# Optimization experiments

Measured on AMD Instinct MI355X. Metric: run time of the kernel, lower is better.

Reference implementation:

```python
import jax, jax.numpy as jnp
import numpy as np

B, S, E, H = 4, 2048, 1024, 16
DK = E // H  # 64


def setup_inputs() -> dict:
    key = jax.random.key(0)
    ks = jax.random.split(key, 11)
    s_in = 1.0 / np.sqrt(E)
    return {
        "query": jax.random.normal(ks[0], (B, S, E), jnp.float32),
        "key_": jax.random.normal(ks[1], (B, S, E), jnp.float32),
        "value": jax.random.normal(ks[2], (B, S, E), jnp.float32),
        # nn.Linear weights stored as [out, in]; applied as x @ W.T + b
        "Wq": jax.random.uniform(ks[3], (E, E), jnp.float32, -s_in, s_in),
        "bq": jax.random.uniform(ks[4], (E,), jnp.float32, -s_in, s_in),
        "Wk": jax.random.uniform(ks[5], (E, E), jnp.float32, -s_in, s_in),
        "bk": jax.random.uniform(ks[6], (E,), jnp.float32, -s_in, s_in),
        "Wv": jax.random.uniform(ks[7], (E, E), jnp.float32, -s_in, s_in),
        "bv": jax.random.uniform(ks[8], (E,), jnp.float32, -s_in, s_in),
        "Wo": jax.random.uniform(ks[9], (E, E), jnp.float32, -s_in, s_in),
        "bo": jax.random.uniform(ks[10], (E,), jnp.float32, -s_in, s_in),
    }


def reference(query, key_, value, Wq, bq, Wk, bk, Wv, bv, Wo, bo):
    scale = 1.0 / np.sqrt(DK).astype(np.float32)
    Q = query @ Wq.T + bq   # [B,S,E]
    K = key_ @ Wk.T + bk
    V = value @ Wv.T + bv
    # split heads: [B,S,H,DK] (slicing dim -1 into contiguous per-head chunks)
    Qh = Q.reshape(B, S, H, DK)
    Kh = K.reshape(B, S, H, DK)
    Vh = V.reshape(B, S, H, DK)
    scores = jnp.einsum('bqhd,bkhd->bhqk', Qh, Kh) * scale  # [B,H,S,S]
    probs = jax.nn.softmax(scores, axis=-1)
    ctx = jnp.einsum('bhqk,bkhd->bqhd', probs, Vh).reshape(B, S, E)
    out = ctx @ Wo.T + bo
    return out
```

## Files before the change

kernel.cpp:

```cpp
#include <hip/hip_runtime.h>
#include <stdint.h>
#include <stddef.h>

constexpr int BB = 4, SS = 2048, EE = 1024, HH = 16, DKH = 64;
constexpr int MM = BB * SS;
constexpr float SM_SCALE_LOG2 = 0.18033688011112042f;

typedef unsigned short u16;
typedef __attribute__((ext_vector_type(8))) short bf16x8;
typedef __attribute__((ext_vector_type(8))) unsigned short u16x8;
typedef __attribute__((ext_vector_type(4))) float f32x4;
typedef __attribute__((ext_vector_type(16))) float f32x16;
typedef __attribute__((ext_vector_type(2))) unsigned int u32x2;
typedef __attribute__((ext_vector_type(4))) unsigned int u32x4;

__device__ __forceinline__ u16 f2bf(float f) {
  unsigned u = __builtin_bit_cast(unsigned, f);
  u += 0x7FFFu + ((u >> 16) & 1u);
  return (u16)(u >> 16);
}

__device__ __forceinline__ unsigned pack2(float lo, float hi) {
  unsigned r;
  asm("v_cvt_pk_bf16_f32 %0, %1, %2" : "=v"(r) : "v"(lo), "v"(hi));
  return r;
}

__device__ __forceinline__ void gld16(const void* g, void* l) {
  __builtin_amdgcn_global_load_lds(
      (const __attribute__((address_space(1))) unsigned int*)g,
      (__attribute__((address_space(3))) unsigned int*)l, 16, 0, 0);
}

struct Cvt3 { const float* in[3]; u16* out[3]; };
struct Cvt4 { const float* in[4]; u16* out[4]; };

__global__ void cvt_bf16_x3(Cvt3 p, int n8) {
  int i = blockIdx.x * 256 + threadIdx.x;
  if (i >= n8) return;
  const int z = blockIdx.y;
  const float4* src = (const float4*)p.in[z] + (size_t)i * 2;
  float4 a = src[0], b = src[1];
  u16x8 v;
  v[0] = f2bf(a.x); v[1] = f2bf(a.y); v[2] = f2bf(a.z); v[3] = f2bf(a.w);
  v[4] = f2bf(b.x); v[5] = f2bf(b.y); v[6] = f2bf(b.z); v[7] = f2bf(b.w);
  *((u16x8*)p.out[z] + i) = v;
}

__global__ void cvt_bf16_x4(Cvt4 p, int n8) {
  int i = blockIdx.x * 256 + threadIdx.x;
  if (i >= n8) return;
  const int z = blockIdx.y;
  const float4* src = (const float4*)p.in[z] + (size_t)i * 2;
  float4 a = src[0], b = src[1];
  u16x8 v;
  v[0] = f2bf(a.x); v[1] = f2bf(a.y); v[2] = f2bf(a.z); v[3] = f2bf(a.w);
  v[4] = f2bf(b.x); v[5] = f2bf(b.y); v[6] = f2bf(b.z); v[7] = f2bf(b.w);
  *((u16x8*)p.out[z] + i) = v;
}

struct GemmPtrs {
  const u16* A[3];
  const u16* W[3];
  const float* bias[3];
  void* C[3];
  float scale[3];
  int mode[3];
};

__global__ __launch_bounds__(256, 2) void gemm_bt(GemmPtrs p, int M, int N, int K) {
  __shared__ __align__(16) u16 As[2][128 * 32];
  __shared__ __align__(16) u16 Bs[2][128 * 32];
  const int t = threadIdx.x, l = t & 63, w = t >> 6;
  const int lm = l & 15, lg = l >> 4;
  const int wm = w >> 1, wn = w & 1;
  const int z = blockIdx.z;
  const u16* A = p.A[z];
  const u16* W = p.W[z];
  const float* bias = p.bias[z];
  const int m0 = blockIdx.y * 128, n0 = blockIdx.x * 128;
  const int wbase = (t & ~63) * 16;

  f32x4 acc[4][4];
  const f32x4 zero = {0.f, 0.f, 0.f, 0.f};
#pragma unroll
  for (int i = 0; i < 4; ++i)
#pragma unroll
    for (int j = 0; j < 4; ++j) acc[i][j] = zero;

  auto stage = [&](int buf, int kt) {
    const int k0 = kt * 32;
#pragma unroll
    for (int i = 0; i < 2; ++i) {
      const int slot = i * 256 + t;
      const int row = slot >> 2, c = slot & 3;
      gld16(A + (size_t)(m0 + row) * K + k0 + c * 8, (char*)&As[buf][0] + i * 4096 + wbase);
      gld16(W + (size_t)(n0 + row) * K + k0 + c * 8, (char*)&Bs[buf][0] + i * 4096 + wbase);
    }
  };

  stage(0, 0);
  __syncthreads();
  int cur = 0;
  const int NT = K >> 5;
  for (int kt = 0; kt < NT; ++kt) {
    if (kt + 1 < NT) stage(cur ^ 1, kt + 1);
    const u16* Ac = &As[cur][0];
    const u16* Bc = &Bs[cur][0];
    bf16x8 a[4], b[4];
#pragma unroll
    for (int i = 0; i < 4; ++i)
      a[i] = *(const bf16x8*)(Ac + (wm * 64 + i * 16 + lm) * 32 + lg * 8);
#pragma unroll
    for (int j = 0; j < 4; ++j)
      b[j] = *(const bf16x8*)(Bc + (wn * 64 + j * 16 + lm) * 32 + lg * 8);
#pragma unroll
    for (int i = 0; i < 4; ++i)
#pragma unroll
      for (int j = 0; j < 4; ++j)
        acc[i][j] = __builtin_amdgcn_mfma_f32_16x16x32_bf16(a[i], b[j], acc[i][j], 0, 0, 0);
    __syncthreads();
    cur ^= 1;
  }

  const float sc = p.scale[z];
  const int mode = p.mode[z];
#pragma unroll
  for (int i = 0; i < 4; ++i) {
    const int rbase = m0 + wm * 64 + i * 16 + lg * 4;
#pragma unroll
    for (int j = 0; j < 4; ++j) {
      const int col = n0 + wn * 64 + j * 16 + lm;
      const float bv = bias[col];
      float v[4];
#pragma unroll
      for (int r = 0; r < 4; ++r) v[r] = (acc[i][j][r] + bv) * sc;
      if (mode == 1) {
#pragma unroll
        for (int r = 0; r < 4; ++r)
          ((float*)p.C[z])[(size_t)(rbase + r) * N + col] = v[r];
      } else if (mode == 0) {
#pragma unroll
        for (int r = 0; r < 4; ++r)
          ((u16*)p.C[z])[(size_t)(rbase + r) * N + col] = f2bf(v[r]);
      } else {
        const int b = rbase >> 11, s = rbase & 2047;
        u16* dst = (u16*)p.C[z] +
                   ((size_t)((b * 16 + (col >> 6)) * 64 + (col & 63))) * SS + s;
        uint2 pk;
        pk.x = pack2(v[0], v[1]);
        pk.y = pack2(v[2], v[3]);
        *(uint2*)dst = pk;
      }
    }
  }
}

__global__ __launch_bounds__(256, 4) void attn_fwd3(const u16* __restrict__ Q,
                                                    const u16* __restrict__ K,
                                                    const u16* __restrict__ Vt,
                                                    u16* __restrict__ C) {
  __shared__ __align__(16) u16 Ks[2][64 * 64];
  __shared__ __align__(16) u16 Vs[2][64 * 64];

  const int t = threadIdx.x, l = t & 63, w = t >> 6;
  const int lq = l & 31, hi = l >> 5;
  const int q0 = blockIdx.x * 128;
  const int bh = blockIdx.y, bb = bh >> 4, hh = bh & 15;

  const u16* qp = Q + ((size_t)(bb * SS + q0 + w * 32 + lq)) * EE + hh * 64 + hi * 8;
  bf16x8 qf[4];
  qf[0] = *(const bf16x8*)(qp);
  qf[1] = *(const bf16x8*)(qp + 16);
  qf[2] = *(const bf16x8*)(qp + 32);
  qf[3] = *(const bf16x8*)(qp + 48);

  const u16* Kbase = K + (size_t)bb * SS * EE + hh * 64;
  const u16* Vbase = Vt + (size_t)bh * DKH * SS;

  f32x16 accA, accB;
  f32x16 z16;
#pragma unroll
  for (int i = 0; i < 16; ++i) { accA[i] = 0.f; accB[i] = 0.f; z16[i] = 0.f; }
  float lsum = 0.0f;

  auto stage = [&](int buf, int kt) {
#pragma unroll
    for (int i = 0; i < 2; ++i) {
      const int slot = i * 256 + t;
      const int row = slot >> 3, pc = slot & 7;
      const int lc = pc ^ (row & 7);
      const int lbyte = (i * 256 + (t & ~63)) * 16;
      gld16(Kbase + (size_t)(kt * 64 + row) * EE + lc * 8, (char*)&Ks[buf][0] + lbyte);
      gld16(Vbase + (size_t)row * SS + kt * 64 + lc * 8, (char*)&Vs[buf][0] + lbyte);
    }
  };

  auto mkfrag = [&](const f32x16& p, int base) -> bf16x8 {
    unsigned A0 = pack2(p[base + 0], p[base + 1]);
    unsigned A1 = pack2(p[base + 2], p[base + 3]);
    unsigned B0 = pack2(p[base + 4], p[base + 5]);
    unsigned B1 = pack2(p[base + 6], p[base + 7]);
    u32x2 r0 = __builtin_amdgcn_permlane32_swap(A0, B0, false, false);
    u32x2 r1 = __builtin_amdgcn_permlane32_swap(A1, B1, false, false);
    u32x4 fr;
    fr[0] = r0[0]; fr[1] = r1[0]; fr[2] = r0[1]; fr[3] = r1[1];
    return __builtin_bit_cast(bf16x8, fr);
  };

  stage(0, 0);
  __syncthreads();
  int cur = 0;
  for (int kt = 0; kt < SS / 64; ++kt) {
    if (kt + 1 < SS / 64) stage(cur ^ 1, kt + 1);
    const u16* Kc = &Ks[cur][0];
    const u16* Vc = &Vs[cur][0];

    f32x16 s0, s1;
    __builtin_amdgcn_s_setprio(1);
    {
      const int c = hi ^ (lq & 7);
      bf16x8 kf0 = *(const bf16x8*)(Kc + lq * 64 + c * 8);
      bf16x8 kf1 = *(const bf16x8*)(Kc + (32 + lq) * 64 + c * 8);
      s0 = __builtin_amdgcn_mfma_f32_32x32x16_bf16(kf0, qf[0], z16, 0, 0, 0);
      s1 = __builtin_amdgcn_mfma_f32_32x32x16_bf16(kf1, qf[0], z16, 0, 0, 0);
    }
#pragma unroll
    for (int m = 1; m < 4; ++m) {
      const int c = (2 * m + hi) ^ (lq & 7);
      bf16x8 kf0 = *(const bf16x8*)(Kc + lq * 64 + c * 8);
      bf16x8 kf1 = *(const bf16x8*)(Kc + (32 + lq) * 64 + c * 8);
      s0 = __builtin_amdgcn_mfma_f32_32x32x16_bf16(kf0, qf[m], s0, 0, 0, 0);
      s1 = __builtin_amdgcn_mfma_f32_32x32x16_bf16(kf1, qf[m], s1, 0, 0, 0);
    }
    __builtin_amdgcn_s_setprio(0);

#pragma unroll
    for (int i = 0; i < 16; ++i) {
      s0[i] = __builtin_amdgcn_exp2f(s0[i]);
      s1[i] = __builtin_amdgcn_exp2f(s1[i]);
    }
    float sa = 0.f, sb = 0.f, sc2 = 0.f, sd = 0.f;
#pragma unroll
    for (int i = 0; i < 8; ++i) {
      sa += s0[i]; sb += s0[i + 8];
      sc2 += s1[i]; sd += s1[i + 8];
    }
    lsum += (sa + sb) + (sc2 + sd);

    bf16x8 pf[4];
    pf[0] = mkfrag(s0, 0);
    pf[1] = mkfrag(s0, 8);
    pf[2] = mkfrag(s1, 0);
    pf[3] = mkfrag(s1, 8);

    __builtin_amdgcn_s_setprio(1);
#pragma unroll
    for (int s = 0; s < 4; ++s) {
      const int c = (2 * s + hi) ^ (lq & 7);
      bf16x8 vf0 = *(const bf16x8*)(Vc + lq * 64 + c * 8);
      bf16x8 vf1 = *(const bf16x8*)(Vc + (32 + lq) * 64 + c * 8);
      accA = __builtin_amdgcn_mfma_f32_32x32x16_bf16(vf0, pf[s], accA, 0, 0, 0);
      accB = __builtin_amdgcn_mfma_f32_32x32x16_bf16(vf1, pf[s], accB, 0, 0, 0);
    }
    __builtin_amdgcn_s_setprio(0);
    __syncthreads();
    cur ^= 1;
  }

  const float inv = 1.0f / (lsum + __shfl_xor(lsum, 32));
  char* Tw = (char*)&Ks[0][0] + w * 4096;
#pragma unroll
  for (int g = 0; g < 4; ++g) {
    uint2 pa, pb;
    pa.x = pack2(accA[4 * g + 0] * inv, accA[4 * g + 1] * inv);
    pa.y = pack2(accA[4 * g + 2] * inv, accA[4 * g + 3] * inv);
    pb.x = pack2(accB[4 * g + 0] * inv, accB[4 * g + 1] * inv);
    pb.y = pack2(accB[4 * g + 2] * inv, accB[4 * g + 3] * inv);
    const int sub = 8 * hi, sw = (lq & 7) << 4;
    *(uint2*)(Tw + lq * 128 + (((g) << 4) ^ sw) + sub) = pa;
    *(uint2*)(Tw + lq * 128 + (((4 + g) << 4) ^ sw) + sub) = pb;
  }
  const int qr0 = l >> 3, ch = l & 7;
#pragma unroll
  for (int ps = 0; ps < 4; ++ps) {
    const int qr = ps * 8 + qr0;
    u32x4 vv = *(const u32x4*)(Tw + qr * 128 + ((ch ^ (qr & 7)) << 4));
    u16* dst = C + ((size_t)(bb * SS + q0 + w * 32 + qr)) * EE + hh * 64 + ch * 8;
    *(u32x4*)dst = vv;
  }
}

extern "C" void kernel_launch(void* const* d_in, const int* in_sizes, int n_in,
                              void* d_out, int out_size, void* d_ws, size_t ws_size,
                              hipStream_t stream) {
  (void)in_sizes; (void)n_in; (void)out_size; (void)ws_size;
  const float* query = (const float*)d_in[0];
  const float* key_  = (const float*)d_in[1];
  const float* value = (const float*)d_in[2];
  const float* Wq = (const float*)d_in[3];
  const float* bq = (const float*)d_in[4];
  const float* Wk = (const float*)d_in[5];
  const float* bk = (const float*)d_in[6];
  const float* Wv = (const float*)d_in[7];
  const float* bv = (const float*)d_in[8];
  const float* Wo = (const float*)d_in[9];
  const float* bo = (const float*)d_in[10];

  char* ws = (char*)d_ws;
  const size_t SZX = (size_t)MM * EE * 2;
  const size_t SZW = (size_t)EE * EE * 2;
  u16* Xq  = (u16*)(ws + 0 * SZX);
  u16* Xk  = (u16*)(ws + 1 * SZX);
  u16* Xv  = (u16*)(ws + 2 * SZX);
  u16* Qb  = (u16*)(ws + 3 * SZX);
  u16* Kb  = (u16*)(ws + 4 * SZX);
  u16* Vtb = (u16*)(ws + 5 * SZX);
  u16* Cb  = (u16*)(ws + 6 * SZX);
  u16* Wqb = (u16*)(ws + 7 * SZX + 0 * SZW);
  u16* Wkb = (u16*)(ws + 7 * SZX + 1 * SZW);
  u16* Wvb = (u16*)(ws + 7 * SZX + 2 * SZW);
  u16* Wob = (u16*)(ws + 7 * SZX + 3 * SZW);

  const int n8x = MM * EE / 8;
  const int n8w = EE * EE / 8;

  Cvt3 cx{};
  cx.in[0] = query; cx.in[1] = key_; cx.in[2] = value;
  cx.out[0] = Xq; cx.out[1] = Xk; cx.out[2] = Xv;
  cvt_bf16_x3<<<dim3(n8x / 256, 3), 256, 0, stream>>>(cx, n8x);

  Cvt4 cw{};
  cw.in[0] = Wq; cw.in[1] = Wk; cw.in[2] = Wv; cw.in[3] = Wo;
  cw.out[0] = Wqb; cw.out[1] = Wkb; cw.out[2] = Wvb; cw.out[3] = Wob;
  cvt_bf16_x4<<<dim3(n8w / 256, 4), 256, 0, stream>>>(cw, n8w);

  GemmPtrs g{};
  g.A[0] = Xq; g.A[1] = Xk; g.A[2] = Xv;
  g.W[0] = Wqb; g.W[1] = Wkb; g.W[2] = Wvb;
  g.bias[0] = bq; g.bias[1] = bk; g.bias[2] = bv;
  g.C[0] = Qb; g.C[1] = Kb; g.C[2] = Vtb;
  g.scale[0] = SM_SCALE_LOG2; g.scale[1] = 1.0f; g.scale[2] = 1.0f;
  g.mode[0] = 0; g.mode[1] = 0; g.mode[2] = 2;
  gemm_bt<<<dim3(EE / 128, MM / 128, 3), 256, 0, stream>>>(g, MM, EE, EE);

  attn_fwd3<<<dim3(SS / 128, BB * HH), 256, 0, stream>>>(Qb, Kb, Vtb, Cb);

  GemmPtrs g2{};
  g2.A[0] = Cb; g2.W[0] = Wob; g2.bias[0] = bo; g2.C[0] = d_out;
  g2.scale[0] = 1.0f; g2.mode[0] = 1;
  gemm_bt<<<dim3(EE / 128, MM / 128, 1), 256, 0, stream>>>(g2, MM, EE, EE);
}
```

Before: 224.9 us.

## Replace projection GEMM with 256x256 tile, triple-buffered, swizzled LDS kernel

```diff
diff --git a/kernel.cpp b/kernel.cpp
--- a/kernel.cpp
+++ b/kernel.cpp
@@ -68,23 +68,29 @@
   int mode[3];
 };
 
-__global__ __launch_bounds__(256, 2) void gemm_bt(GemmPtrs p, int M, int N, int K) {
-  __shared__ __align__(16) u16 As[2][128 * 32];
-  __shared__ __align__(16) u16 Bs[2][128 * 32];
-  const int t = threadIdx.x, l = t & 63, w = t >> 6;
+__global__ __launch_bounds__(512, 2) void gemm256(GemmPtrs p, int M, int N, int K) {
+  __shared__ __align__(16) u16 SA[3][256 * 32];
+  __shared__ __align__(16) u16 SB[3][256 * 32];
+  const int t = threadIdx.x, l = t & 63;
+  const int w = t >> 6;
   const int lm = l & 15, lg = l >> 4;
-  const int wm = w >> 1, wn = w & 1;
+  const int wm = w >> 2, wn = w & 3;
   const int z = blockIdx.z;
   const u16* A = p.A[z];
   const u16* W = p.W[z];
   const float* bias = p.bias[z];
-  const int m0 = blockIdx.y * 128, n0 = blockIdx.x * 128;
-  const int wbase = (t & ~63) * 16;
-
-  f32x4 acc[4][4];
+
+  const int nwg = gridDim.x * gridDim.y;
+  const int o = blockIdx.y * gridDim.x + blockIdx.x;
+  const int cpx = nwg >> 3;
+  const int sw = (o & 7) * cpx + (o >> 3);
+  const int n0 = (sw % gridDim.x) * 256;
+  const int m0 = (sw / gridDim.x) * 256;
+
+  f32x4 acc[8][4];
   const f32x4 zero = {0.f, 0.f, 0.f, 0.f};
 #pragma unroll
-  for (int i = 0; i < 4; ++i)
+  for (int i = 0; i < 8; ++i)
 #pragma unroll
     for (int j = 0; j < 4; ++j) acc[i][j] = zero;
 
@@ -92,42 +98,55 @@
     const int k0 = kt * 32;
 #pragma unroll
     for (int i = 0; i < 2; ++i) {
-      const int slot = i * 256 + t;
-      const int row = slot >> 2, c = slot & 3;
-      gld16(A + (size_t)(m0 + row) * K + k0 + c * 8, (char*)&As[buf][0] + i * 4096 + wbase);
-      gld16(W + (size_t)(n0 + row) * K + k0 + c * 8, (char*)&Bs[buf][0] + i * 4096 + wbase);
+      const int cidx = i * 512 + t;
+      const int row = cidx >> 2, pc = cidx & 3;
+      const int lc = pc ^ (row & 3);
+      const int dstoff = (i * 512 + (t & ~63)) * 16;
+      gld16(A + (size_t)(m0 + row) * K + k0 + lc * 8, (char*)&SA[buf][0] + dstoff);
+      gld16(W + (size_t)(n0 + row) * K + k0 + lc * 8, (char*)&SB[buf][0] + dstoff);
     }
   };
 
   stage(0, 0);
-  __syncthreads();
-  int cur = 0;
+  stage(1, 1);
+  int cb = 0;
   const int NT = K >> 5;
+  const int rsw = (lg ^ (lm & 3)) * 8;
   for (int kt = 0; kt < NT; ++kt) {
-    if (kt + 1 < NT) stage(cur ^ 1, kt + 1);
-    const u16* Ac = &As[cur][0];
-    const u16* Bc = &Bs[cur][0];
-    bf16x8 a[4], b[4];
-#pragma unroll
-    for (int i = 0; i < 4; ++i)
-      a[i] = *(const bf16x8*)(Ac + (wm * 64 + i * 16 + lm) * 32 + lg * 8);
+    if (kt == NT - 1)
+      asm volatile("s_waitcnt vmcnt(0)" ::: "memory");
+    else
+      asm volatile("s_waitcnt vmcnt(4)" ::: "memory");
+    __builtin_amdgcn_s_barrier();
+    const u16* Ac = &SA[cb][0];
+    const u16* Bc = &SB[cb][0];
+    bf16x8 a[8], b[4];
+#pragma unroll
+    for (int i = 0; i < 8; ++i)
+      a[i] = *(const bf16x8*)(Ac + (wm * 128 + i * 16 + lm) * 32 + rsw);
 #pragma unroll
     for (int j = 0; j < 4; ++j)
-      b[j] = *(const bf16x8*)(Bc + (wn * 64 + j * 16 + lm) * 32 + lg * 8);
-#pragma unroll
-    for (int i = 0; i < 4; ++i)
+      b[j] = *(const bf16x8*)(Bc + (wn * 64 + j * 16 + lm) * 32 + rsw);
+    if (kt + 2 < NT) {
+      int sb = cb + 2;
+      if (sb >= 3) sb -= 3;
+      stage(sb, kt + 2);
+    }
+    __builtin_amdgcn_s_setprio(1);
+#pragma unroll
+    for (int i = 0; i < 8; ++i)
 #pragma unroll
       for (int j = 0; j < 4; ++j)
         acc[i][j] = __builtin_amdgcn_mfma_f32_16x16x32_bf16(a[i], b[j], acc[i][j], 0, 0, 0);
-    __syncthreads();
-    cur ^= 1;
+    __builtin_amdgcn_s_setprio(0);
+    cb = (cb == 2) ? 0 : cb + 1;
   }
 
   const float sc = p.scale[z];
   const int mode = p.mode[z];
 #pragma unroll
-  for (int i = 0; i < 4; ++i) {
-    const int rbase = m0 + wm * 64 + i * 16 + lg * 4;
+  for (int i = 0; i < 8; ++i) {
+    const int rbase = m0 + wm * 128 + i * 16 + lg * 4;
 #pragma unroll
     for (int j = 0; j < 4; ++j) {
       const int col = n0 + wn * 64 + j * 16 + lm;
@@ -342,12 +361,12 @@
   g.C[0] = Qb; g.C[1] = Kb; g.C[2] = Vtb;
   g.scale[0] = SM_SCALE_LOG2; g.scale[1] = 1.0f; g.scale[2] = 1.0f;
   g.mode[0] = 0; g.mode[1] = 0; g.mode[2] = 2;
-  gemm_bt<<<dim3(EE / 128, MM / 128, 3), 256, 0, stream>>>(g, MM, EE, EE);
+  gemm256<<<dim3(EE / 256, MM / 256, 3), 512, 0, stream>>>(g, MM, EE, EE);
 
   attn_fwd3<<<dim3(SS / 128, BB * HH), 256, 0, stream>>>(Qb, Kb, Vtb, Cb);
 
   GemmPtrs g2{};
   g2.A[0] = Cb; g2.W[0] = Wob; g2.bias[0] = bo; g2.C[0] = d_out;
   g2.scale[0] = 1.0f; g2.mode[0] = 1;
-  gemm_bt<<<dim3(EE / 128, MM / 128, 1), 256, 0, stream>>>(g2, MM, EE, EE);
-}
+  gemm256<<<dim3(EE / 256, MM / 256, 1), 512, 0, stream>>>(g2, MM, EE, EE);
+}
```

Measured after the change: 219.0 us. 2.6% less time.

## Rewrite projection GEMM with 32x32 MFMA, swizzled LDS and block remap

Applied to the files above, without the earlier changes.

```diff
diff --git a/kernel.cpp b/kernel.cpp
--- a/kernel.cpp
+++ b/kernel.cpp
@@ -68,34 +68,42 @@
   int mode[3];
 };
 
-__global__ __launch_bounds__(256, 2) void gemm_bt(GemmPtrs p, int M, int N, int K) {
-  __shared__ __align__(16) u16 As[2][128 * 32];
-  __shared__ __align__(16) u16 Bs[2][128 * 32];
+__global__ __launch_bounds__(256, 4) void gemm32(GemmPtrs p, int M, int N, int K) {
+  __shared__ __align__(16) u16 SA[2][64 * 64];
+  __shared__ __align__(16) u16 SB[2][64 * 64];
   const int t = threadIdx.x, l = t & 63, w = t >> 6;
-  const int lm = l & 15, lg = l >> 4;
+  const int lq = l & 31, hi = l >> 5;
   const int wm = w >> 1, wn = w & 1;
   const int z = blockIdx.z;
   const u16* A = p.A[z];
   const u16* W = p.W[z];
   const float* bias = p.bias[z];
-  const int m0 = blockIdx.y * 128, n0 = blockIdx.x * 128;
-  const int wbase = (t & ~63) * 16;
-
-  f32x4 acc[4][4];
-  const f32x4 zero = {0.f, 0.f, 0.f, 0.f};
-#pragma unroll
-  for (int i = 0; i < 4; ++i)
-#pragma unroll
-    for (int j = 0; j < 4; ++j) acc[i][j] = zero;
+
+  const int nwg = gridDim.x * gridDim.y;
+  const int o = blockIdx.y * gridDim.x + blockIdx.x;
+  const int sw = (o & 7) * (nwg >> 3) + (o >> 3);
+  const int n0 = (sw % gridDim.x) * 128;
+  const int m0 = (sw / gridDim.x) * 128;
+
+  f32x16 acc[2][2];
+#pragma unroll
+  for (int i = 0; i < 2; ++i)
+#pragma unroll
+    for (int j = 0; j < 2; ++j)
+#pragma unroll
+      for (int r = 0; r < 16; ++r) acc[i][j][r] = 0.f;
 
   auto stage = [&](int buf, int kt) {
-    const int k0 = kt * 32;
 #pragma unroll
     for (int i = 0; i < 2; ++i) {
-      const int slot = i * 256 + t;
-      const int row = slot >> 2, c = slot & 3;
-      gld16(A + (size_t)(m0 + row) * K + k0 + c * 8, (char*)&As[buf][0] + i * 4096 + wbase);
-      gld16(W + (size_t)(n0 + row) * K + k0 + c * 8, (char*)&Bs[buf][0] + i * 4096 + wbase);
+      const int ci = i * 256 + t;
+      const int r = ci >> 3, P = ci & 7;
+      const int L = P ^ (r & 7);
+      const int m = r + ((L & 4) << 4);
+      const int kc = L & 3;
+      const int dst = (i * 256 + (t & ~63)) * 16;
+      gld16(A + (size_t)(m0 + m) * K + kt * 32 + kc * 8, (char*)&SA[buf][0] + dst);
+      gld16(W + (size_t)(n0 + m) * K + kt * 32 + kc * 8, (char*)&SB[buf][0] + dst);
     }
   };
 
@@ -103,22 +111,26 @@
   __syncthreads();
   int cur = 0;
   const int NT = K >> 5;
+  const int lsw = lq & 7;
   for (int kt = 0; kt < NT; ++kt) {
     if (kt + 1 < NT) stage(cur ^ 1, kt + 1);
-    const u16* Ac = &As[cur][0];
-    const u16* Bc = &Bs[cur][0];
-    bf16x8 a[4], b[4];
-#pragma unroll
-    for (int i = 0; i < 4; ++i)
-      a[i] = *(const bf16x8*)(Ac + (wm * 64 + i * 16 + lm) * 32 + lg * 8);
-#pragma unroll
-    for (int j = 0; j < 4; ++j)
-      b[j] = *(const bf16x8*)(Bc + (wn * 64 + j * 16 + lm) * 32 + lg * 8);
-#pragma unroll
-    for (int i = 0; i < 4; ++i)
-#pragma unroll
-      for (int j = 0; j < 4; ++j)
-        acc[i][j] = __builtin_amdgcn_mfma_f32_16x16x32_bf16(a[i], b[j], acc[i][j], 0, 0, 0);
+    const u16* Ac = &SA[cur][0];
+    const u16* Bc = &SB[cur][0];
+    __builtin_amdgcn_s_setprio(1);
+#pragma unroll
+    for (int ks = 0; ks < 2; ++ks) {
+      const int ca = ((wm << 2) + (ks << 1) + hi) ^ lsw;
+      const int cb = ((wn << 2) + (ks << 1) + hi) ^ lsw;
+      bf16x8 a0 = *(const bf16x8*)(Ac + lq * 64 + ca * 8);
+      bf16x8 a1 = *(const bf16x8*)(Ac + (32 + lq) * 64 + ca * 8);
+      bf16x8 b0 = *(const bf16x8*)(Bc + lq * 64 + cb * 8);
+      bf16x8 b1 = *(const bf16x8*)(Bc + (32 + lq) * 64 + cb * 8);
+      acc[0][0] = __builtin_amdgcn_mfma_f32_32x32x16_bf16(a0, b0, acc[0][0], 0, 0, 0);
+      acc[0][1] = __builtin_amdgcn_mfma_f32_32x32x16_bf16(a0, b1, acc[0][1], 0, 0, 0);
+      acc[1][0] = __builtin_amdgcn_mfma_f32_32x32x16_bf16(a1, b0, acc[1][0], 0, 0, 0);
+      acc[1][1] = __builtin_amdgcn_mfma_f32_32x32x16_bf16(a1, b1, acc[1][1], 0, 0, 0);
+    }
+    __builtin_amdgcn_s_setprio(0);
     __syncthreads();
     cur ^= 1;
   }
@@ -126,31 +138,34 @@
   const float sc = p.scale[z];
   const int mode = p.mode[z];
 #pragma unroll
-  for (int i = 0; i < 4; ++i) {
-    const int rbase = m0 + wm * 64 + i * 16 + lg * 4;
-#pragma unroll
-    for (int j = 0; j < 4; ++j) {
-      const int col = n0 + wn * 64 + j * 16 + lm;
+  for (int fr = 0; fr < 2; ++fr) {
+#pragma unroll
+    for (int fc = 0; fc < 2; ++fc) {
+      const int col = n0 + wn * 64 + fc * 32 + lq;
       const float bv = bias[col];
-      float v[4];
-#pragma unroll
-      for (int r = 0; r < 4; ++r) v[r] = (acc[i][j][r] + bv) * sc;
-      if (mode == 1) {
-#pragma unroll
-        for (int r = 0; r < 4; ++r)
-          ((float*)p.C[z])[(size_t)(rbase + r) * N + col] = v[r];
-      } else if (mode == 0) {
-#pragma unroll
-        for (int r = 0; r < 4; ++r)
-          ((u16*)p.C[z])[(size_t)(rbase + r) * N + col] = f2bf(v[r]);
-      } else {
-        const int b = rbase >> 11, s = rbase & 2047;
-        u16* dst = (u16*)p.C[z] +
-                   ((size_t)((b * 16 + (col >> 6)) * 64 + (col & 63))) * SS + s;
-        uint2 pk;
-        pk.x = pack2(v[0], v[1]);
-        pk.y = pack2(v[2], v[3]);
-        *(uint2*)dst = pk;
+#pragma unroll
+      for (int g = 0; g < 4; ++g) {
+        const int mb = m0 + wm * 64 + fr * 32 + 8 * g + 4 * hi;
+        float v[4];
+#pragma unroll
+        for (int j = 0; j < 4; ++j) v[j] = (acc[fr][fc][4 * g + j] + bv) * sc;
+        if (mode == 1) {
+#pragma unroll
+          for (int j = 0; j < 4; ++j)
+            ((float*)p.C[z])[(size_t)(mb + j) * N + col] = v[j];
+        } else if (mode == 0) {
+#pragma unroll
+          for (int j = 0; j < 4; ++j)
+            ((u16*)p.C[z])[(size_t)(mb + j) * N + col] = f2bf(v[j]);
+        } else {
+          const int b = mb >> 11, s = mb & 2047;
+          u16* dst = (u16*)p.C[z] +
+                     ((size_t)((b * 16 + (col >> 6)) * 64 + (col & 63))) * SS + s;
+          uint2 pk;
+          pk.x = pack2(v[0], v[1]);
+          pk.y = pack2(v[2], v[3]);
+          *(uint2*)dst = pk;
+        }
       }
     }
   }
@@ -342,12 +357,12 @@
   g.C[0] = Qb; g.C[1] = Kb; g.C[2] = Vtb;
   g.scale[0] = SM_SCALE_LOG2; g.scale[1] = 1.0f; g.scale[2] = 1.0f;
   g.mode[0] = 0; g.mode[1] = 0; g.mode[2] = 2;
-  gemm_bt<<<dim3(EE / 128, MM / 128, 3), 256, 0, stream>>>(g, MM, EE, EE);
+  gemm32<<<dim3(EE / 128, MM / 128, 3), 256, 0, stream>>>(g, MM, EE, EE);
 
   attn_fwd3<<<dim3(SS / 128, BB * HH), 256, 0, stream>>>(Qb, Kb, Vtb, Cb);
 
   GemmPtrs g2{};
   g2.A[0] = Cb; g2.W[0] = Wob; g2.bias[0] = bo; g2.C[0] = d_out;
   g2.scale[0] = 1.0f; g2.mode[0] = 1;
-  gemm_bt<<<dim3(EE / 128, MM / 128, 1), 256, 0, stream>>>(g2, MM, EE, EE);
-}
+  gemm32<<<dim3(EE / 128, MM / 128, 1), 256, 0, stream>>>(g2, MM, EE, EE);
+}
```

New measurement: 211.8 us. 5.8% less time.

## Enlarge GEMM tile to 256x128 with swizzled LDS and grid remap

Applied to the files above, without the earlier changes.

```diff
diff --git a/kernel.cpp b/kernel.cpp
--- a/kernel.cpp
+++ b/kernel.cpp
@@ -68,9 +68,9 @@
   int mode[3];
 };
 
-__global__ __launch_bounds__(256, 2) void gemm_bt(GemmPtrs p, int M, int N, int K) {
-  __shared__ __align__(16) u16 As[2][128 * 32];
-  __shared__ __align__(16) u16 Bs[2][128 * 32];
+__global__ __launch_bounds__(256, 2) void gemm128(GemmPtrs p, int M, int N, int K) {
+  __shared__ __align__(16) u16 SA[2][128 * 64];
+  __shared__ __align__(16) u16 SB[2][64 * 64];
   const int t = threadIdx.x, l = t & 63, w = t >> 6;
   const int lm = l & 15, lg = l >> 4;
   const int wm = w >> 1, wn = w & 1;
@@ -78,24 +78,41 @@
   const u16* A = p.A[z];
   const u16* W = p.W[z];
   const float* bias = p.bias[z];
-  const int m0 = blockIdx.y * 128, n0 = blockIdx.x * 128;
-  const int wbase = (t & ~63) * 16;
-
-  f32x4 acc[4][4];
+
+  const int nwg = gridDim.x * gridDim.y;
+  const int o = blockIdx.y * gridDim.x + blockIdx.x;
+  const int sw = (o & 7) * (nwg >> 3) + (o >> 3);
+  const int n0 = (sw % gridDim.x) * 128;
+  const int m0 = (sw / gridDim.x) * 256;
+
+  f32x4 acc[8][4];
   const f32x4 zero = {0.f, 0.f, 0.f, 0.f};
 #pragma unroll
-  for (int i = 0; i < 4; ++i)
+  for (int i = 0; i < 8; ++i)
 #pragma unroll
     for (int j = 0; j < 4; ++j) acc[i][j] = zero;
 
   auto stage = [&](int buf, int kt) {
     const int k0 = kt * 32;
 #pragma unroll
+    for (int i = 0; i < 4; ++i) {
+      const int ci = i * 256 + t;
+      const int r = ci >> 3, P = ci & 7;
+      const int L = P ^ (r & 7);
+      const int mr = r + ((L & 4) << 5);
+      const int kc = L & 3;
+      gld16(A + (size_t)(m0 + mr) * K + k0 + kc * 8,
+            (char*)&SA[buf][0] + (i * 256 + (t & ~63)) * 16);
+    }
+#pragma unroll
     for (int i = 0; i < 2; ++i) {
-      const int slot = i * 256 + t;
-      const int row = slot >> 2, c = slot & 3;
-      gld16(A + (size_t)(m0 + row) * K + k0 + c * 8, (char*)&As[buf][0] + i * 4096 + wbase);
-      gld16(W + (size_t)(n0 + row) * K + k0 + c * 8, (char*)&Bs[buf][0] + i * 4096 + wbase);
+      const int ci = i * 256 + t;
+      const int r = ci >> 3, P = ci & 7;
+      const int L = P ^ (r & 7);
+      const int mr = r + ((L & 4) << 4);
+      const int kc = L & 3;
+      gld16(W + (size_t)(n0 + mr) * K + k0 + kc * 8,
+            (char*)&SB[buf][0] + (i * 256 + (t & ~63)) * 16);
     }
   };
 
@@ -103,22 +120,27 @@
   __syncthreads();
   int cur = 0;
   const int NT = K >> 5;
+  const int lsw = lm & 7;
   for (int kt = 0; kt < NT; ++kt) {
     if (kt + 1 < NT) stage(cur ^ 1, kt + 1);
-    const u16* Ac = &As[cur][0];
-    const u16* Bc = &Bs[cur][0];
-    bf16x8 a[4], b[4];
-#pragma unroll
-    for (int i = 0; i < 4; ++i)
-      a[i] = *(const bf16x8*)(Ac + (wm * 64 + i * 16 + lm) * 32 + lg * 8);
-#pragma unroll
-    for (int j = 0; j < 4; ++j)
-      b[j] = *(const bf16x8*)(Bc + (wn * 64 + j * 16 + lm) * 32 + lg * 8);
-#pragma unroll
-    for (int i = 0; i < 4; ++i)
-#pragma unroll
-      for (int j = 0; j < 4; ++j)
-        acc[i][j] = __builtin_amdgcn_mfma_f32_16x16x32_bf16(a[i], b[j], acc[i][j], 0, 0, 0);
+    const u16* Ac = &SA[cur][0];
+    const u16* Bc = &SB[cur][0];
+    const int pa = ((lg + 4 * wm) ^ lsw) * 8;
+    const int pb = ((lg + 4 * wn) ^ lsw) * 8;
+    bf16x8 a[8], b[4];
+#pragma unroll
+    for (int fi = 0; fi < 8; ++fi)
+      a[fi] = *(const bf16x8*)(Ac + (fi * 16 + lm) * 64 + pa);
+#pragma unroll
+    for (int fj = 0; fj < 4; ++fj)
+      b[fj] = *(const bf16x8*)(Bc + (fj * 16 + lm) * 64 + pb);
+    __builtin_amdgcn_s_setprio(1);
+#pragma unroll
+    for (int fi = 0; fi < 8; ++fi)
+#pragma unroll
+      for (int fj = 0; fj < 4; ++fj)
+        acc[fi][fj] = __builtin_amdgcn_mfma_f32_16x16x32_bf16(a[fi], b[fj], acc[fi][fj], 0, 0, 0);
+    __builtin_amdgcn_s_setprio(0);
     __syncthreads();
     cur ^= 1;
   }
@@ -126,15 +148,15 @@
   const float sc = p.scale[z];
   const int mode = p.mode[z];
 #pragma unroll
-  for (int i = 0; i < 4; ++i) {
-    const int rbase = m0 + wm * 64 + i * 16 + lg * 4;
-#pragma unroll
-    for (int j = 0; j < 4; ++j) {
-      const int col = n0 + wn * 64 + j * 16 + lm;
+  for (int fi = 0; fi < 8; ++fi) {
+    const int rbase = m0 + wm * 128 + fi * 16 + lg * 4;
+#pragma unroll
+    for (int fj = 0; fj < 4; ++fj) {
+      const int col = n0 + wn * 64 + fj * 16 + lm;
       const float bv = bias[col];
       float v[4];
 #pragma unroll
-      for (int r = 0; r < 4; ++r) v[r] = (acc[i][j][r] + bv) * sc;
+      for (int r = 0; r < 4; ++r) v[r] = (acc[fi][fj][r] + bv) * sc;
       if (mode == 1) {
 #pragma unroll
         for (int r = 0; r < 4; ++r)
@@ -144,9 +166,9 @@
         for (int r = 0; r < 4; ++r)
           ((u16*)p.C[z])[(size_t)(rbase + r) * N + col] = f2bf(v[r]);
       } else {
-        const int b = rbase >> 11, s = rbase & 2047;
+        const int b2 = rbase >> 11, s = rbase & 2047;
         u16* dst = (u16*)p.C[z] +
-                   ((size_t)((b * 16 + (col >> 6)) * 64 + (col & 63))) * SS + s;
+                   ((size_t)((b2 * 16 + (col >> 6)) * 64 + (col & 63))) * SS + s;
         uint2 pk;
         pk.x = pack2(v[0], v[1]);
         pk.y = pack2(v[2], v[3]);
@@ -342,12 +364,12 @@
   g.C[0] = Qb; g.C[1] = Kb; g.C[2] = Vtb;
   g.scale[0] = SM_SCALE_LOG2; g.scale[1] = 1.0f; g.scale[2] = 1.0f;
   g.mode[0] = 0; g.mode[1] = 0; g.mode[2] = 2;
-  gemm_bt<<<dim3(EE / 128, MM / 128, 3), 256, 0, stream>>>(g, MM, EE, EE);
+  gemm128<<<dim3(EE / 128, MM / 256, 3), 256, 0, stream>>>(g, MM, EE, EE);
 
   attn_fwd3<<<dim3(SS / 128, BB * HH), 256, 0, stream>>>(Qb, Kb, Vtb, Cb);
 
   GemmPtrs g2{};
   g2.A[0] = Cb; g2.W[0] = Wob; g2.bias[0] = bo; g2.C[0] = d_out;
   g2.scale[0] = 1.0f; g2.mode[0] = 1;
-  gemm_bt<<<dim3(EE / 128, MM / 128, 1), 256, 0, stream>>>(g2, MM, EE, EE);
-}
+  gemm128<<<dim3(EE / 128, MM / 256, 1), 256, 0, stream>>>(g2, MM, EE, EE);
+}
```

Measured after the change: 231.6 us. 1.03x slower.
